# Optimization experiments

Hardware: AMD Instinct MI355X
Metric: run time of the kernel (lower is better)

The kernel has to match this reference:

```python
import jax, jax.numpy as jnp
import numpy as np

SEGMENT_LENGTHS = [2048, 4096, 8192]
DILATION_RATES = [1, 2, 4]
BATCH, SEQ_LEN, HEADS, HEAD_DIM = 1, 8192, 16, 64
SCALE = HEAD_DIM ** (-0.5)


def _hilbert_index_to_xy(index, n):
    # Exact replica of the torch module's integer Hilbert d->(x,y) mapping.
    x = y = 0
    s = 1
    while s < n:
        rx = 1 & (index // 2)
        ry = 1 & (index ^ rx)
        if ry == 0:
            if rx == 1:
                x, y = s - 1 - y, s - 1 - x
            x, y = y, x
        x += s * rx
        y += s * ry
        index //= 4
        s *= 2
    return x, y


def _hilbert_perm(n):
    # Replicates _generate_hilbert_indices, including the fill-in tail and
    d = 1
    while d * d < n:
        d *= 2
    idx = []
    for i in range(min(n, d * d)):
        x, y = _hilbert_index_to_xy(i, d)
        p = x * d + y
        if p < n:
            idx.append(p)
    if len(idx) < n:
        idx.extend(range(len(idx), n))
    perm = np.array(idx[:n], dtype=np.int64)
    inv = np.zeros(n, dtype=np.int64)
    inv[perm] = np.arange(n, dtype=np.int64)
    return perm, inv


_PERM_CACHE = {}


def _get_perm(n):
    if n not in _PERM_CACHE:
        _PERM_CACHE[n] = _hilbert_perm(n)
    return _PERM_CACHE[n]


def setup_inputs() -> dict:
    key = jax.random.key(0)
    kq, kk, kv = jax.random.split(key, 3)
    shape = (BATCH, SEQ_LEN, HEADS, HEAD_DIM)
    return {
        "q": jax.random.normal(kq, shape, dtype=jnp.float32),
        "k": jax.random.normal(kk, shape, dtype=jnp.float32),
        "v": jax.random.normal(kv, shape, dtype=jnp.float32),
    }


def reference(q, k, v) -> jnp.ndarray:
    B, L, H, D = q.shape
    n_groups = len(SEGMENT_LENGTHS)
    heads_per_group = max(1, H // n_groups)
    out = jnp.zeros_like(q)
    for g, (seg_len, dil) in enumerate(zip(SEGMENT_LENGTHS, DILATION_RATES)):
        S = min(seg_len, L)
        h0 = g * heads_per_group
        if h0 >= H:
            continue
        h1 = min(h0 + heads_per_group, H)
        assert L % S == 0, "seq_len must tile into segments"
        N = L // S  # number of segments
        Hg = h1 - h0
        # [B, N, S, Hg, D]
        qg = q[:, :, h0:h1].reshape(B, N, S, Hg, D)
        kg = k[:, :, h0:h1].reshape(B, N, S, Hg, D)
        vg = v[:, :, h0:h1].reshape(B, N, S, Hg, D)
        if S > 64:
            perm, inv = _get_perm(S)
        else:
            perm = np.arange(S, dtype=np.int64)
            inv = perm
        # dilation applied AFTER Hilbert ordering -> compose the gathers
        kv_idx = perm[np.arange(0, S, dil)]
        qp = qg[:, :, perm]           # [B,N,S,Hg,D]
        kd = kg[:, :, kv_idx]         # [B,N,S/dil,Hg,D]
        vd = vg[:, :, kv_idx]
        scores = jnp.einsum('bnqhd,bnkhd->bnhqk', qp, kd) * SCALE
        attn = jnp.nan_to_num(jax.nn.softmax(scores, axis=-1))
        og = jnp.einsum('bnhqk,bnkhd->bnqhd', attn, vd)  # [B,N,S,Hg,D]
        og = og[:, :, inv]            # inverse Hilbert scatter
        out = out.at[:, :, h0:h1].set(og.reshape(B, L, Hg, D))
    return out
```

## Files before the change

### kernel.cpp

```cpp
#include <hip/hip_runtime.h>
#include <hip/hip_bf16.h>

typedef __attribute__((ext_vector_type(8))) short bf16x8;
typedef __attribute__((ext_vector_type(16))) float f32x16;
typedef __attribute__((ext_vector_type(2))) unsigned u32x2;

__device__ __forceinline__ unsigned pk2(float a, float b) {
    union { __hip_bfloat162 h2; unsigned u; } c;
    c.h2 = __float22bfloat162_rn(make_float2(a, b));
    return c.u;
}

__device__ __forceinline__ void gld16(const void* g, void* l) {
    __builtin_amdgcn_global_load_lds(
        (const __attribute__((address_space(1))) unsigned*)g,
        (__attribute__((address_space(3))) unsigned*)l, 16, 0, 0);
}

__device__ inline int hilbert_p(int index, int d) {
    int x = 0, y = 0;
    for (int s = 1; s < d; s <<= 1) {
        int rx = (index >> 1) & 1;
        int ry = (index ^ rx) & 1;
        if (ry == 0) {
            if (rx == 1) {
                int nx = s - 1 - y;
                int ny = s - 1 - x;
                x = nx; y = ny;
            }
            int t = x; x = y; y = t;
        }
        x += s * rx;
        y += s * ry;
        index >>= 2;
    }
    return x * d + y;
}

__global__ __launch_bounds__(256, 4) void gather_kv(
    const float* __restrict__ K, const float* __restrict__ V,
    short* __restrict__ Kp, short* __restrict__ Vp)
{
    const int b = blockIdx.x;
    int g, rb;
    if (b < 640)      { g = 0; rb = b; }
    else if (b < 960) { g = 1; rb = b - 640; }
    else              { g = 2; rb = b - 960; }
    const int nseg   = 4 >> g;
    const int hl     = rb / (nseg * 32);
    const int r2     = rb - hl * (nseg * 32);
    const int seg    = r2 >> 5;
    const int kt     = r2 & 31;
    const int h      = g * 5 + hl;
    const int S      = 2048 << g;
    const int segrow = seg * S;
    const int dgrid  = (g == 2) ? 128 : 64;
    const size_t tile_s = (size_t)b * 4096;

    const int tid = threadIdx.x;

    if (tid < 64) {
        const int k8 = tid >> 3;
        const int d8 = tid & 7;
        float rowf[8][8];
#pragma unroll
        for (int u = 0; u < 8; ++u) {
            const int j  = k8 * 8 + u;
            const int ii = kt * 64 + j;
            const int p  = (g == 0) ? ii : hilbert_p(ii << g, dgrid);
            const float* vp = V + ((size_t)((segrow + p) * 16 + h)) * 64 + d8 * 8;
            float4 a = ((const float4*)vp)[0];
            float4 bq = ((const float4*)vp)[1];
            rowf[u][0] = a.x;  rowf[u][1] = a.y;  rowf[u][2] = a.z;  rowf[u][3] = a.w;
            rowf[u][4] = bq.x; rowf[u][5] = bq.y; rowf[u][6] = bq.z; rowf[u][7] = bq.w;
        }
#pragma unroll
        for (int w = 0; w < 8; ++w) {
            const int dd = d8 * 8 + w;
            union { unsigned u4[4]; bf16x8 v; } o;
            o.u4[0] = pk2(rowf[0][w], rowf[1][w]);
            o.u4[1] = pk2(rowf[2][w], rowf[3][w]);
            o.u4[2] = pk2(rowf[4][w], rowf[5][w]);
            o.u4[3] = pk2(rowf[6][w], rowf[7][w]);
            const int vchunk = ((k8 >> 1) * 2 + (dd >> 5)) * 64 + (k8 & 1) * 32 + (dd & 31);
            *(bf16x8*)&Vp[tile_s + vchunk * 8] = o.v;
        }
    } else {
        for (int it = tid - 64; it < 512; it += 192) {
            const int j  = it >> 3;
            const int c8 = it & 7;
            const int ii = kt * 64 + j;
            const int p  = (g == 0) ? ii : hilbert_p(ii << g, dgrid);
            const float* kp = K + ((size_t)((segrow + p) * 16 + h)) * 64 + c8 * 8;
            float4 k0 = ((const float4*)kp)[0];
            float4 k1 = ((const float4*)kp)[1];
            union { unsigned u4[4]; bf16x8 v; } ck;
            ck.u4[0] = pk2(k0.x, k0.y); ck.u4[1] = pk2(k0.z, k0.w);
            ck.u4[2] = pk2(k1.x, k1.y); ck.u4[3] = pk2(k1.z, k1.w);
            const int kchunk = ((j >> 5) * 4 + (c8 >> 1)) * 64 + (c8 & 1) * 32 + (j & 31);
            *(bf16x8*)&Kp[tile_s + kchunk * 8] = ck.v;
        }
    }
}

__global__ __launch_bounds__(256, 4) void attn_kernel(
    const float* __restrict__ Q, float* __restrict__ O,
    const short* __restrict__ Kp, const short* __restrict__ Vp)
{
    __shared__ __align__(16) short ldsK[2][4096];
    __shared__ __align__(16) short ldsV[2][4096];

    const int bx = blockIdx.x;
    const int g  = bx / 320;
    const int r  = bx - g * 320;
    const int hl = r >> 6;
    const int qb = r & 63;
    const int h  = g * 5 + hl;
    const int qglob = qb * 128;
    const int seg   = qb >> (4 + g);
    const int tile0 = ((g == 0) ? 0 : (g == 1) ? 640 : 960) + (hl * (4 >> g) + seg) * 32;

    const int tid  = threadIdx.x;
    const int wave = tid >> 6;
    const int lane = tid & 63;
    const int l31  = lane & 31;
    const int hi   = lane >> 5;

    if (g == 0 && hl == 0) {
        const float4 z = make_float4(0.f, 0.f, 0.f, 0.f);
        for (int i = tid; i < 2048; i += 256) {
            int row = qglob + (i >> 4);
            ((float4*)O)[(size_t)(row * 16 + 15) * 16 + (i & 15)] = z;
        }
    }

    const float cs = 0.125f * 1.44269504088896f;
    bf16x8 qf[4];
    {
        const int qrow = qglob + wave * 32 + l31;
        const float* qp = Q + ((size_t)(qrow * 16 + h)) * 64;
#pragma unroll
        for (int ks = 0; ks < 4; ++ks) {
            const float4* p4 = (const float4*)(qp + ks * 16 + hi * 8);
            float4 a = p4[0], b = p4[1];
            union { unsigned u[4]; bf16x8 v; } f;
            f.u[0] = pk2(a.x * cs, a.y * cs); f.u[1] = pk2(a.z * cs, a.w * cs);
            f.u[2] = pk2(b.x * cs, b.y * cs); f.u[3] = pk2(b.z * cs, b.w * cs);
            qf[ks] = f.v;
        }
    }

    f32x16 oacc[2];
#pragma unroll
    for (int rr = 0; rr < 16; ++rr) { oacc[0][rr] = 0.f; oacc[1][rr] = 0.f; }
    float lp = 0.f;

    const int lbase = lane * 8;

    {
        const size_t tb = (size_t)tile0 << 13;
        const char* kgp = (const char*)Kp + tb + (wave << 11) + (lane << 4);
        const char* vgp = (const char*)Vp + tb + (wave << 11) + (lane << 4);
        char* klp = (char*)&ldsK[0][0] + (wave << 11);
        char* vlp = (char*)&ldsV[0][0] + (wave << 11);
        gld16(kgp,        klp);
        gld16(kgp + 1024, klp + 1024);
        gld16(vgp,        vlp);
        gld16(vgp + 1024, vlp + 1024);
    }

    for (int kt = 0; kt < 32; ++kt) {
        const int cur = kt & 1;
        if (kt < 31) {
            const size_t tb = (size_t)(tile0 + kt + 1) << 13;
            const char* kgp = (const char*)Kp + tb + (wave << 11) + (lane << 4);
            const char* vgp = (const char*)Vp + tb + (wave << 11) + (lane << 4);
            char* klp = (char*)&ldsK[cur ^ 1][0] + (wave << 11);
            char* vlp = (char*)&ldsV[cur ^ 1][0] + (wave << 11);
            gld16(kgp,        klp);
            gld16(kgp + 1024, klp + 1024);
            gld16(vgp,        vlp);
            gld16(vgp + 1024, vlp + 1024);
            asm volatile("s_waitcnt vmcnt(4)" ::: "memory");
        } else {
            asm volatile("s_waitcnt vmcnt(0)" ::: "memory");
        }
        asm volatile("s_barrier" ::: "memory");

        const short* lK = &ldsK[cur][lbase];
        const short* lV = &ldsV[cur][lbase];

        float lacc = 0.f;
        unsigned dw[16];
        __builtin_amdgcn_s_setprio(1);
#pragma unroll
        for (int kb = 0; kb < 2; ++kb) {
            bf16x8 kf0 = *(const bf16x8*)&lK[(kb * 4 + 0) * 512];
            bf16x8 kf1 = *(const bf16x8*)&lK[(kb * 4 + 1) * 512];
            bf16x8 kf2 = *(const bf16x8*)&lK[(kb * 4 + 2) * 512];
            bf16x8 kf3 = *(const bf16x8*)&lK[(kb * 4 + 3) * 512];
            f32x16 sa;
#pragma unroll
            for (int rr = 0; rr < 16; ++rr) sa[rr] = 0.f;
            sa = __builtin_amdgcn_mfma_f32_32x32x16_bf16(kf0, qf[0], sa, 0, 0, 0);
            sa = __builtin_amdgcn_mfma_f32_32x32x16_bf16(kf1, qf[1], sa, 0, 0, 0);
            sa = __builtin_amdgcn_mfma_f32_32x32x16_bf16(kf2, qf[2], sa, 0, 0, 0);
            sa = __builtin_amdgcn_mfma_f32_32x32x16_bf16(kf3, qf[3], sa, 0, 0, 0);
            float pe[16];
#pragma unroll
            for (int rr = 0; rr < 16; ++rr) pe[rr] = __builtin_amdgcn_exp2f(sa[rr]);
            lacc += (((pe[0] + pe[1]) + (pe[2] + pe[3])) + ((pe[4] + pe[5]) + (pe[6] + pe[7])))
                  + (((pe[8] + pe[9]) + (pe[10] + pe[11])) + ((pe[12] + pe[13]) + (pe[14] + pe[15])));
#pragma unroll
            for (int kslo = 0; kslo < 2; ++kslo)
#pragma unroll
                for (int j = 0; j < 2; ++j)
#pragma unroll
                    for (int hT = 0; hT < 2; ++hT) {
                        const int r0 = 2 * j + 8 * kslo + 4 * hT;
                        dw[(kb * 2 + kslo) * 4 + j * 2 + hT] = pk2(pe[r0], pe[r0 + 1]);
                    }
        }
        __builtin_amdgcn_s_setprio(0);
        lp += lacc;

        bf16x8 pa[4];
#pragma unroll
        for (int ks = 0; ks < 4; ++ks) {
            u32x2 r0 = __builtin_amdgcn_permlane32_swap(dw[ks * 4 + 0], dw[ks * 4 + 1], false, false);
            u32x2 r1 = __builtin_amdgcn_permlane32_swap(dw[ks * 4 + 2], dw[ks * 4 + 3], false, false);
            union { unsigned u[4]; bf16x8 v; } p;
            p.u[0] = r0[0]; p.u[1] = r1[0]; p.u[2] = r0[1]; p.u[3] = r1[1];
            pa[ks] = p.v;
        }

        __builtin_amdgcn_sched_barrier(0);

        bf16x8 vf[4][2];
#pragma unroll
        for (int ks = 0; ks < 4; ++ks)
#pragma unroll
            for (int db = 0; db < 2; ++db)
                vf[ks][db] = *(const bf16x8*)&lV[(ks * 2 + db) * 512];

        __builtin_amdgcn_s_setprio(1);
#pragma unroll
        for (int ks = 0; ks < 4; ++ks) {
            oacc[0] = __builtin_amdgcn_mfma_f32_32x32x16_bf16(pa[ks], vf[ks][0], oacc[0], 0, 0, 0);
            oacc[1] = __builtin_amdgcn_mfma_f32_32x32x16_bf16(pa[ks], vf[ks][1], oacc[1], 0, 0, 0);
        }
        __builtin_amdgcn_s_setprio(0);

        asm volatile("s_barrier" ::: "memory");
    }

    float ltot = lp + __shfl_xor(lp, 32, 64);
    float linv = 1.0f / ltot;

#pragma unroll
    for (int rr = 0; rr < 16; ++rr) {
        const int m = (rr & 3) + ((rr >> 2) << 3) + (hi << 2);
        float inv = __shfl(linv, m, 64);
        const int qrow = qglob + wave * 32 + m;
        float* op = O + ((size_t)(qrow * 16 + h)) * 64 + l31;
        op[0]  = oacc[0][rr] * inv;
        op[32] = oacc[1][rr] * inv;
    }
}

extern "C" void kernel_launch(void* const* d_in, const int* in_sizes, int n_in,
                              void* d_out, int out_size, void* d_ws, size_t ws_size,
                              hipStream_t stream) {
    const float* q = (const float*)d_in[0];
    const float* k = (const float*)d_in[1];
    const float* v = (const float*)d_in[2];
    float* out = (float*)d_out;
    short* Kp = (short*)d_ws;
    short* Vp = Kp + (size_t)1120 * 4096;

    gather_kv<<<1120, 256, 0, stream>>>(k, v, Kp, Vp);
    attn_kernel<<<960, 256, 0, stream>>>(q, out, Kp, Vp);
}
```

Baseline: 207.8 us.

## Fuse KV gather and attention into one cooperative kernel with grid sync

Merges the K/V gather-and-convert pass and the attention kernel into a single cooperative launch of 960 blocks. The gather work is spread as a grid-stride loop over all threads, followed by a threadfence and a grid-wide barrier before attention runs, so one kernel launch and its tail gap go away. The V gather is also restructured: each thread now reads eight scalar floats with a strided pattern instead of vector loads, which may coalesce worse. If the cooperative launch fails, it falls back to two separate launches.

```diff
diff --git a/kernel.cpp b/kernel.cpp
--- a/kernel.cpp
+++ b/kernel.cpp
@@ -1,5 +1,8 @@
 #include <hip/hip_runtime.h>
 #include <hip/hip_bf16.h>
+#include <hip/hip_cooperative_groups.h>
+
+namespace cg = cooperative_groups;
 
 typedef __attribute__((ext_vector_type(8))) short bf16x8;
 typedef __attribute__((ext_vector_type(16))) float f32x16;
@@ -37,73 +40,61 @@
     return x * d + y;
 }
 
-__global__ __launch_bounds__(256, 4) void gather_kv(
-    const float* __restrict__ K, const float* __restrict__ V,
-    short* __restrict__ Kp, short* __restrict__ Vp)
-{
-    const int b = blockIdx.x;
+struct TileGeo { int g, h, segrow, dgrid, kt; };
+__device__ __forceinline__ TileGeo tile_decode(int b) {
+    TileGeo t;
     int g, rb;
     if (b < 640)      { g = 0; rb = b; }
     else if (b < 960) { g = 1; rb = b - 640; }
     else              { g = 2; rb = b - 960; }
-    const int nseg   = 4 >> g;
-    const int hl     = rb / (nseg * 32);
-    const int r2     = rb - hl * (nseg * 32);
-    const int seg    = r2 >> 5;
-    const int kt     = r2 & 31;
-    const int h      = g * 5 + hl;
-    const int S      = 2048 << g;
-    const int segrow = seg * S;
-    const int dgrid  = (g == 2) ? 128 : 64;
-    const size_t tile_s = (size_t)b * 4096;
-
-    const int tid = threadIdx.x;
-
-    if (tid < 64) {
-        const int k8 = tid >> 3;
-        const int d8 = tid & 7;
-        float rowf[8][8];
-#pragma unroll
-        for (int u = 0; u < 8; ++u) {
-            const int j  = k8 * 8 + u;
-            const int ii = kt * 64 + j;
-            const int p  = (g == 0) ? ii : hilbert_p(ii << g, dgrid);
-            const float* vp = V + ((size_t)((segrow + p) * 16 + h)) * 64 + d8 * 8;
-            float4 a = ((const float4*)vp)[0];
-            float4 bq = ((const float4*)vp)[1];
-            rowf[u][0] = a.x;  rowf[u][1] = a.y;  rowf[u][2] = a.z;  rowf[u][3] = a.w;
-            rowf[u][4] = bq.x; rowf[u][5] = bq.y; rowf[u][6] = bq.z; rowf[u][7] = bq.w;
-        }
-#pragma unroll
-        for (int w = 0; w < 8; ++w) {
-            const int dd = d8 * 8 + w;
-            union { unsigned u4[4]; bf16x8 v; } o;
-            o.u4[0] = pk2(rowf[0][w], rowf[1][w]);
-            o.u4[1] = pk2(rowf[2][w], rowf[3][w]);
-            o.u4[2] = pk2(rowf[4][w], rowf[5][w]);
-            o.u4[3] = pk2(rowf[6][w], rowf[7][w]);
-            const int vchunk = ((k8 >> 1) * 2 + (dd >> 5)) * 64 + (k8 & 1) * 32 + (dd & 31);
-            *(bf16x8*)&Vp[tile_s + vchunk * 8] = o.v;
-        }
-    } else {
-        for (int it = tid - 64; it < 512; it += 192) {
-            const int j  = it >> 3;
-            const int c8 = it & 7;
-            const int ii = kt * 64 + j;
-            const int p  = (g == 0) ? ii : hilbert_p(ii << g, dgrid);
-            const float* kp = K + ((size_t)((segrow + p) * 16 + h)) * 64 + c8 * 8;
-            float4 k0 = ((const float4*)kp)[0];
-            float4 k1 = ((const float4*)kp)[1];
-            union { unsigned u4[4]; bf16x8 v; } ck;
-            ck.u4[0] = pk2(k0.x, k0.y); ck.u4[1] = pk2(k0.z, k0.w);
-            ck.u4[2] = pk2(k1.x, k1.y); ck.u4[3] = pk2(k1.z, k1.w);
-            const int kchunk = ((j >> 5) * 4 + (c8 >> 1)) * 64 + (c8 & 1) * 32 + (j & 31);
-            *(bf16x8*)&Kp[tile_s + kchunk * 8] = ck.v;
-        }
-    }
-}
-
-__global__ __launch_bounds__(256, 4) void attn_kernel(
+    const int nseg = 4 >> g;
+    const int hl   = rb / (nseg * 32);
+    const int r2   = rb - hl * (nseg * 32);
+    t.g      = g;
+    t.h      = g * 5 + hl;
+    t.kt     = r2 & 31;
+    t.segrow = (r2 >> 5) * (2048 << g);
+    t.dgrid  = (g == 2) ? 128 : 64;
+    return t;
+}
+
+__device__ __forceinline__ void k_item(int i, const float* __restrict__ K,
+                                       short* __restrict__ Kp) {
+    const int tile = i >> 9, idx = i & 511;
+    const int j = idx >> 3, c8 = idx & 7;
+    const TileGeo t = tile_decode(tile);
+    const int ii = t.kt * 64 + j;
+    const int p  = (t.g == 0) ? ii : hilbert_p(ii << t.g, t.dgrid);
+    const float* kp = K + ((size_t)((t.segrow + p) * 16 + t.h)) * 64 + c8 * 8;
+    float4 k0 = ((const float4*)kp)[0];
+    float4 k1 = ((const float4*)kp)[1];
+    union { unsigned u4[4]; bf16x8 v; } ck;
+    ck.u4[0] = pk2(k0.x, k0.y); ck.u4[1] = pk2(k0.z, k0.w);
+    ck.u4[2] = pk2(k1.x, k1.y); ck.u4[3] = pk2(k1.z, k1.w);
+    const int kchunk = ((j >> 5) * 4 + (c8 >> 1)) * 64 + (c8 & 1) * 32 + (j & 31);
+    *(bf16x8*)&Kp[(size_t)tile * 4096 + kchunk * 8] = ck.v;
+}
+
+__device__ __forceinline__ void v_item(int i, const float* __restrict__ V,
+                                       short* __restrict__ Vp) {
+    const int tile = i >> 9, idx = i & 511;
+    const int k8 = idx >> 6, dd = idx & 63;
+    const TileGeo t = tile_decode(tile);
+    float rv[8];
+#pragma unroll
+    for (int u = 0; u < 8; ++u) {
+        const int ii = t.kt * 64 + k8 * 8 + u;
+        const int p  = (t.g == 0) ? ii : hilbert_p(ii << t.g, t.dgrid);
+        rv[u] = V[((size_t)((t.segrow + p) * 16 + t.h)) * 64 + dd];
+    }
+    union { unsigned u4[4]; bf16x8 v; } o;
+    o.u4[0] = pk2(rv[0], rv[1]); o.u4[1] = pk2(rv[2], rv[3]);
+    o.u4[2] = pk2(rv[4], rv[5]); o.u4[3] = pk2(rv[6], rv[7]);
+    const int vchunk = ((k8 >> 1) * 2 + (dd >> 5)) * 64 + (k8 & 1) * 32 + (dd & 31);
+    *(bf16x8*)&Vp[(size_t)tile * 4096 + vchunk * 8] = o.v;
+}
+
+__device__ __forceinline__ void attn_body(
     const float* __restrict__ Q, float* __restrict__ O,
     const short* __restrict__ Kp, const short* __restrict__ Vp)
 {
@@ -268,6 +259,37 @@
     }
 }
 
+__global__ __launch_bounds__(256, 4) void fused_kernel(
+    const float* __restrict__ Q, float* __restrict__ O,
+    const float* __restrict__ K, const float* __restrict__ V,
+    short* __restrict__ Kp, short* __restrict__ Vp)
+{
+    const int gt   = blockIdx.x * 256 + threadIdx.x;
+    const int step = gridDim.x * 256;
+    for (int i = gt; i < 1120 * 512; i += step) k_item(i, K, Kp);
+    for (int i = gt; i < 1120 * 512; i += step) v_item(i, V, Vp);
+    __threadfence();
+    cg::this_grid().sync();
+    attn_body(Q, O, Kp, Vp);
+}
+
+__global__ __launch_bounds__(256, 4) void gather_kv(
+    const float* __restrict__ K, const float* __restrict__ V,
+    short* __restrict__ Kp, short* __restrict__ Vp)
+{
+    const int gt   = blockIdx.x * 256 + threadIdx.x;
+    const int step = gridDim.x * 256;
+    for (int i = gt; i < 1120 * 512; i += step) k_item(i, K, Kp);
+    for (int i = gt; i < 1120 * 512; i += step) v_item(i, V, Vp);
+}
+
+__global__ __launch_bounds__(256, 4) void attn_kernel(
+    const float* __restrict__ Q, float* __restrict__ O,
+    const short* __restrict__ Kp, const short* __restrict__ Vp)
+{
+    attn_body(Q, O, Kp, Vp);
+}
+
 extern "C" void kernel_launch(void* const* d_in, const int* in_sizes, int n_in,
                               void* d_out, int out_size, void* d_ws, size_t ws_size,
                               hipStream_t stream) {
@@ -278,6 +300,12 @@
     short* Kp = (short*)d_ws;
     short* Vp = Kp + (size_t)1120 * 4096;
 
-    gather_kv<<<1120, 256, 0, stream>>>(k, v, Kp, Vp);
-    attn_kernel<<<960, 256, 0, stream>>>(q, out, Kp, Vp);
-}
+    void* args[] = { (void*)&q, (void*)&out, (void*)&k, (void*)&v,
+                     (void*)&Kp, (void*)&Vp };
+    hipError_t e = hipLaunchCooperativeKernel(
+        (const void*)fused_kernel, dim3(960), dim3(256), args, 0, stream);
+    if (e != hipSuccess) {
+        gather_kv<<<960, 256, 0, stream>>>(k, v, Kp, Vp);
+        attn_kernel<<<960, 256, 0, stream>>>(q, out, Kp, Vp);
+    }
+}
```

New measurement: 352.2 us. 1.69x slower.
